# Performance work log

Hardware: AMD Instinct MI355X
Metric: run time of the kernel (lower is better)

## Reference

```python
import jax, jax.numpy as jnp
import numpy as np

NUM_HEADS = 16

def setup_inputs() -> dict:
    key = jax.random.key(0)
    k1, k2, k3 = jax.random.split(key, 3)
    B, T, C = 4, 2048, 2048
    x = jax.random.normal(k1, (B, T, C), dtype=jnp.float32)
    Wqkv = jax.random.normal(k2, (C, 3 * C), dtype=jnp.float32) * (C ** -0.5)
    bqkv = jnp.zeros((3 * C,), dtype=jnp.float32)
    Wproj = jax.random.normal(k3, (C, C), dtype=jnp.float32) * (C ** -0.5)
    bproj = jnp.zeros((C,), dtype=jnp.float32)
    return {"x": x, "Wqkv": Wqkv, "bqkv": bqkv, "Wproj": Wproj, "bproj": bproj}

def reference(x, Wqkv, bqkv, Wproj, bproj):
    B, T, C = x.shape
    H = NUM_HEADS
    D = C // H  # head_dim
    qkv = x @ Wqkv + bqkv                      # [B,T,3C]
    q, k, v = jnp.split(qkv, 3, axis=-1)
    # [B,T,C] -> [B,H,T,D]
    q = q.reshape(B, T, H, D).transpose(0, 2, 1, 3)
    k = k.reshape(B, T, H, D).transpose(0, 2, 1, 3)
    v = v.reshape(B, T, H, D).transpose(0, 2, 1, 3)
    scale = D ** -0.5
    scores = jnp.einsum('bhqd,bhkd->bhqk', q, k) * scale  # [B,H,T,T]
    causal = jnp.tril(jnp.ones((T, T), dtype=bool))
    scores = jnp.where(causal, scores, jnp.finfo(scores.dtype).min)
    attn = jax.nn.softmax(scores, axis=-1)
    out = jnp.einsum('bhqk,bhkd->bhqd', attn, v)           # [B,H,T,D]
    out = out.transpose(0, 2, 1, 3).reshape(B, T, C)
    return out @ Wproj + bproj
```

## Files before the change

### kernel.cpp

```cpp
#include <hip/hip_runtime.h>
#include <hip/hip_bf16.h>
#include <stdint.h>

typedef __attribute__((ext_vector_type(8))) short short8;
typedef __attribute__((ext_vector_type(4))) float f32x4;
typedef __attribute__((ext_vector_type(16))) float f32x16;
typedef __attribute__((ext_vector_type(2))) unsigned int uint2v;

__device__ __forceinline__ unsigned short f2bf(float f) {
  union { float f; unsigned int u; } v; v.f = f;
  unsigned int r = v.u + 0x7FFFu + ((v.u >> 16) & 1u);
  return (unsigned short)(r >> 16);
}

__device__ __forceinline__ unsigned int cvtpk(float lo, float hi) {
  unsigned int r;
  asm("v_cvt_pk_bf16_f32 %0, %1, %2" : "=v"(r) : "v"(lo), "v"(hi));
  return r;
}

#define GLOAD16(gsrc, ldst)                                                                  \
  __builtin_amdgcn_global_load_lds((const __attribute__((address_space(1))) void*)(gsrc),    \
                                   (__attribute__((address_space(3))) void*)(ldst), 16, 0, 0)

#define BAR() __builtin_amdgcn_s_barrier()
#define LGKMC(n) do { asm volatile("s_waitcnt lgkmcnt(" #n ")" ::: "memory"); \
                      __builtin_amdgcn_sched_barrier(0); } while (0)
#define LGKM0() LGKMC(0)
#define VMCNT0() asm volatile("s_waitcnt vmcnt(0)" ::: "memory")
#define VMCNT8() do { asm volatile("s_waitcnt vmcnt(8)" ::: "memory"); \
                      __builtin_amdgcn_sched_barrier(0); } while (0)
#define PRIO(x) __builtin_amdgcn_s_setprio(x)
#define MFMA16(d, a, b) d = __builtin_amdgcn_mfma_f32_16x16x32_bf16(a, b, d, 0, 0, 0)

__global__ __launch_bounds__(256) void cast_bf16_kernel(const float* __restrict__ in,
                                                        unsigned short* __restrict__ out) {
  int i = blockIdx.x * 256 + threadIdx.x;
  float4 v = ((const float4*)in)[i];
  ushort4 o;
  o.x = f2bf(v.x); o.y = f2bf(v.y); o.z = f2bf(v.z); o.w = f2bf(v.w);
  ((ushort4*)out)[i] = o;
}

__global__ __launch_bounds__(256) void transpose_cast_kernel(const float* __restrict__ W,
                                                             unsigned short* __restrict__ Wt,
                                                             int K, int N) {
  __shared__ float tile[32][33];
  int n0 = blockIdx.x * 32, k0 = blockIdx.y * 32;
  int tx = threadIdx.x, ty = threadIdx.y;
#pragma unroll
  for (int j = 0; j < 32; j += 8)
    tile[ty + j][tx] = W[(size_t)(k0 + ty + j) * N + n0 + tx];
  __syncthreads();
#pragma unroll
  for (int j = 0; j < 32; j += 8)
    Wt[(size_t)(n0 + ty + j) * K + k0 + tx] = f2bf(tile[tx][ty + j]);
}

__device__ __forceinline__ void stage_half(const unsigned short* __restrict__ gp, int K,
                                           int kt, int half, char* lds_mat, int tid) {
#pragma unroll
  for (int it = 0; it < 2; ++it) {
    int li = half * 1024 + it * 512 + tid;
    int r = li >> 3, c = li & 7;
    int cs = c ^ (r & 7);
    GLOAD16(gp + (size_t)r * K + kt * 64 + cs * 8, lds_mat + li * 16);
  }
}

__device__ __forceinline__ void gemm256_mainloop(const unsigned short* __restrict__ Ap,
                                                 const unsigned short* __restrict__ Bp,
                                                 int K, int tid, char* smem,
                                                 f32x4 acc[8][4]) {
  char* sa = smem;
  char* sb = smem + 65536;
  const int KT = K >> 6;

  int wid = tid >> 6, lane = tid & 63;
  int wr = wid >> 2, wc = wid & 3;
  int lg = lane >> 4, l15 = lane & 15;
  int swz7 = l15 & 7;

#define LDA(ab, m, kc) \
  (*(const short8*)((const unsigned short*)(ab) + (size_t)((wr * 128 + (m) * 16 + l15) * 64 + ((((kc) * 4 + lg) ^ swz7) * 8))))
#define LDB(bb, n, kc) \
  (*(const short8*)((const unsigned short*)(bb) + (size_t)((wc * 64 + (n) * 16 + l15) * 64 + ((((kc) * 4 + lg) ^ swz7) * 8))))

  stage_half(Bp, K, 0, 0, sb, tid);
  stage_half(Bp, K, 0, 1, sb, tid);
  stage_half(Ap, K, 0, 0, sa, tid);
  stage_half(Ap, K, 0, 1, sa, tid);
  stage_half(Bp, K, 1, 0, sb + 32768, tid);
  stage_half(Bp, K, 1, 1, sb + 32768, tid);
  stage_half(Ap, K, 1, 0, sa + 32768, tid);
  stage_half(Ap, K, 1, 1, sa + 32768, tid);
  VMCNT8();
  BAR();

  for (int t = 0; t < KT; ++t) {
    int p = t & 1;
    const char* ab = sa + p * 32768;
    const char* bb = sb + p * 32768;
    int kt2 = (t + 2 < KT) ? t + 2 : KT - 1;

    short8 bq01[2][2], bq23[2][2], aq[4][2], aq2[4][2];
#pragma unroll
    for (int n = 0; n < 2; ++n) { bq01[n][0] = LDB(bb, n, 0); bq01[n][1] = LDB(bb, n, 1); }
#pragma unroll
    for (int m = 0; m < 4; ++m) { aq[m][0] = LDA(ab, m, 0); aq[m][1] = LDA(ab, m, 1); }
#pragma unroll
    for (int n = 0; n < 2; ++n) { bq23[n][0] = LDB(bb, n + 2, 0); bq23[n][1] = LDB(bb, n + 2, 1); }
#pragma unroll
    for (int m = 0; m < 4; ++m) { aq2[m][0] = LDA(ab, m + 4, 0); aq2[m][1] = LDA(ab, m + 4, 1); }

    LGKMC(12);
    PRIO(1);
#pragma unroll
    for (int kc = 0; kc < 2; ++kc)
#pragma unroll
      for (int m = 0; m < 4; ++m)
#pragma unroll
        for (int n = 0; n < 2; ++n)
          MFMA16(acc[m][n], aq[m][kc], bq01[n][kc]);
    PRIO(0);

    LGKMC(8);
    BAR();
    stage_half(Bp, K, kt2, 0, sb + p * 32768, tid);
    stage_half(Bp, K, kt2, 1, sb + p * 32768, tid);

    PRIO(1);
#pragma unroll
    for (int kc = 0; kc < 2; ++kc)
#pragma unroll
      for (int m = 0; m < 4; ++m)
#pragma unroll
        for (int n = 0; n < 2; ++n)
          MFMA16(acc[m][n + 2], aq[m][kc], bq23[n][kc]);
    PRIO(0);

    LGKMC(0);
    PRIO(1);
#pragma unroll
    for (int kc = 0; kc < 2; ++kc)
#pragma unroll
      for (int m = 0; m < 4; ++m)
#pragma unroll
        for (int n = 0; n < 2; ++n)
          MFMA16(acc[m + 4][n + 2], aq2[m][kc], bq23[n][kc]);
    PRIO(0);

    BAR();
    stage_half(Ap, K, kt2, 0, sa + p * 32768, tid);
    stage_half(Ap, K, kt2, 1, sa + p * 32768, tid);
    PRIO(1);
#pragma unroll
    for (int kc = 0; kc < 2; ++kc)
#pragma unroll
      for (int m = 0; m < 4; ++m)
#pragma unroll
        for (int n = 0; n < 2; ++n)
          MFMA16(acc[m + 4][n], aq2[m][kc], bq01[n][kc]);
    PRIO(0);
    VMCNT8();
    BAR();
  }
#undef LDA
#undef LDB
}

__global__ __launch_bounds__(512, 2) void gemm_qkv256_kernel(const unsigned short* __restrict__ A,
                                                             const unsigned short* __restrict__ Bt,
                                                             const float* __restrict__ bias,
                                                             unsigned short* __restrict__ qb,
                                                             unsigned short* __restrict__ kb,
                                                             unsigned short* __restrict__ vtb) {
  extern __shared__ char smem[];
  int wg = blockIdx.x;
  int xcd = wg & 7, idx = wg >> 3;
  int bn = xcd * 3 + idx % 3;
  int bm = idx / 3;
  int tid = threadIdx.x;

  f32x4 acc[8][4];
  f32x4 zero = {0.f, 0.f, 0.f, 0.f};
#pragma unroll
  for (int m = 0; m < 8; ++m)
#pragma unroll
    for (int n = 0; n < 4; ++n) acc[m][n] = zero;

  gemm256_mainloop(A + (size_t)bm * 256 * 2048, Bt + (size_t)bn * 256 * 2048, 2048, tid, smem, acc);

  const float QSCALE = (float)(0.08838834764831845 * 1.4426950408889634);
  int wid = tid >> 6, lane = tid & 63;
  int wr = wid >> 2, wc = wid & 3, lg = lane >> 4, l15 = lane & 15;
  int l31 = lane & 31, hi = lane >> 5;

  if (bn >= 16) {
    VMCNT0();
    BAR();
#pragma unroll
    for (int n = 0; n < 4; ++n) {
      int cl = wc * 64 + n * 16 + l15;
      float bv = bias[bn * 256 + cl];
#pragma unroll
      for (int m = 0; m < 8; ++m) {
        int rl = wr * 128 + m * 16 + lg * 4;
        unsigned int w0 = cvtpk(acc[m][n][0] + bv, acc[m][n][1] + bv);
        unsigned int w1 = cvtpk(acc[m][n][2] + bv, acc[m][n][3] + bv);
        uint2v pk = {w0, w1};
        *(uint2v*)(smem + cl * 512 + ((rl * 2) ^ ((cl & 7) << 4))) = pk;
      }
    }
    LGKM0();
    BAR();
    int t0_abs = bm * 256;
    int bq_ = t0_abs >> 11, t0 = t0_abs & 2047;
    int h0 = (bn * 256 - 4096) >> 7;
#pragma unroll
    for (int i = 0; i < 16; ++i) {
      int dloc = i * 16 + wid * 2 + hi;
      short8 vrow = *(const short8*)(smem + dloc * 512 + ((l31 * 16) ^ ((dloc & 7) << 4)));
      int bh_ = bq_ * 16 + h0 + (dloc >> 7);
      int d = dloc & 127;
      *(short8*)(vtb + ((size_t)bh_ * 128 + d) * 2048 + t0 + l31 * 8) = vrow;
    }
  } else {
#pragma unroll
    for (int n = 0; n < 4; ++n) {
      int col = bn * 256 + wc * 64 + n * 16 + l15;
      float bv = bias[col];
      int which = col >> 11;
      int h = (col & 2047) >> 7;
      int d = col & 127;
#pragma unroll
      for (int m = 0; m < 8; ++m) {
#pragma unroll
        for (int g = 0; g < 4; ++g) {
          int row = bm * 256 + wr * 128 + m * 16 + lg * 4 + g;
          int b = row >> 11, t = row & 2047;
          float r = acc[m][n][g] + bv;
          if (which == 0) r *= QSCALE;
          unsigned short val = f2bf(r);
          size_t bhi = (size_t)(b * 16 + h);
          if (which == 0) qb[(bhi * 2048 + t) * 128 + d] = val;
          else            kb[(bhi * 2048 + t) * 128 + d] = val;
        }
      }
    }
  }
}

__global__ __launch_bounds__(512, 2) void gemm_proj256_kernel(const unsigned short* __restrict__ A,
                                                              const unsigned short* __restrict__ Bt,
                                                              const float* __restrict__ bias,
                                                              float* __restrict__ out) {
  extern __shared__ char smem[];
  int wg = blockIdx.x;
  int bm = wg >> 3, bn = wg & 7;
  int tid = threadIdx.x;

  f32x4 acc[8][4];
  f32x4 zero = {0.f, 0.f, 0.f, 0.f};
#pragma unroll
  for (int m = 0; m < 8; ++m)
#pragma unroll
    for (int n = 0; n < 4; ++n) acc[m][n] = zero;

  gemm256_mainloop(A + (size_t)bm * 256 * 2048, Bt + (size_t)bn * 256 * 2048, 2048, tid, smem, acc);

  int wid = tid >> 6, lane = tid & 63;
  int wr = wid >> 2, wc = wid & 3, lg = lane >> 4, l15 = lane & 15;
#pragma unroll
  for (int n = 0; n < 4; ++n) {
    int col = bn * 256 + wc * 64 + n * 16 + l15;
    float bv = bias[col];
#pragma unroll
    for (int m = 0; m < 8; ++m) {
#pragma unroll
      for (int g = 0; g < 4; ++g) {
        int row = bm * 256 + wr * 128 + m * 16 + lg * 4 + g;
        out[(size_t)row * 2048 + col] = acc[m][n][g] + bv;
      }
    }
  }
}

__global__ __launch_bounds__(512) void attn_kernel(const unsigned short* __restrict__ qb,
                                                   const unsigned short* __restrict__ kb,
                                                   const unsigned short* __restrict__ vtb,
                                                   unsigned short* __restrict__ ob) {
  extern __shared__ char asmem[];
  int pairi = blockIdx.x;
  int bh = blockIdx.y;
  int b = bh >> 4, h = bh & 15;
  int tid = threadIdx.x, wid = tid >> 6, lane = tid & 63;
  int l31 = lane & 31, hi = lane >> 5;

  const unsigned short* Q  = qb  + (size_t)bh * 2048 * 128;
  const unsigned short* K  = kb  + (size_t)bh * 2048 * 128;
  const unsigned short* Vt = vtb + (size_t)bh * 128 * 2048;

#pragma unroll 1
  for (int pass = 0; pass < 2; ++pass) {
    int qt = pass == 0 ? (7 - pairi) : pairi;
    int NT = 4 * qt + 4;
    int qbase = qt * 256 + wid * 32;
    int qrow = qbase + l31;

    short8 qf[8];
#pragma unroll
    for (int kc = 0; kc < 8; ++kc)
      qf[kc] = *(const short8*)(Q + (size_t)qrow * 128 + kc * 16 + hi * 8);

    f32x16 o0 = {}, o1 = {}, o2 = {}, o3 = {};
    float m_run = -1e30f, l_run = 0.f;

    {
      char* kb_ = asmem;
#pragma unroll
      for (int it = 0; it < 2; ++it) {
        int li = it * 512 + tid;
        int r = li >> 4, c = li & 15;
        GLOAD16(K + (size_t)r * 128 + (c ^ (r & 7)) * 8, kb_ + li * 16);
      }
#pragma unroll
      for (int it = 0; it < 2; ++it) {
        int li = it * 512 + tid;
        int r = li >> 3, c = li & 7;
        GLOAD16(Vt + (size_t)r * 2048 + (c ^ (r & 7)) * 8, kb_ + 16384 + li * 16);
      }
    }
    VMCNT0();
    BAR();

#pragma unroll 1
    for (int kt = 0; kt < NT; ++kt) {
      char* cb = asmem + ((kt & 1) << 15);
      if (kt + 1 < NT) {
        char* nb = asmem + (((kt + 1) & 1) << 15);
        int kt1 = kt + 1;
#pragma unroll
        for (int it = 0; it < 2; ++it) {
          int li = it * 512 + tid;
          int r = li >> 4, c = li & 15;
          GLOAD16(K + (size_t)(kt1 * 64 + r) * 128 + (c ^ (r & 7)) * 8, nb + li * 16);
        }
#pragma unroll
        for (int it = 0; it < 2; ++it) {
          int li = it * 512 + tid;
          int r = li >> 3, c = li & 7;
          GLOAD16(Vt + (size_t)r * 2048 + kt1 * 64 + (c ^ (r & 7)) * 8, nb + 16384 + li * 16);
        }
      }

      bool active = (kt * 64 <= qbase + 31);
      if (active) {
        const char* k_l = cb;
        const char* v_l = cb + 16384;

        f32x16 s0v = {}, s1v = {};
        PRIO(1);
#pragma unroll
        for (int kc = 0; kc < 8; ++kc) {
          int cg = kc * 2 + hi;
          int sw = l31 & 7;
          short8 kf0 = *(const short8*)(k_l + l31 * 256 + ((cg ^ sw) * 16));
          s0v = __builtin_amdgcn_mfma_f32_32x32x16_bf16(kf0, qf[kc], s0v, 0, 0, 0);
          short8 kf1 = *(const short8*)(k_l + (32 + l31) * 256 + ((cg ^ sw) * 16));
          s1v = __builtin_amdgcn_mfma_f32_32x32x16_bf16(kf1, qf[kc], s1v, 0, 0, 0);
        }
        PRIO(0);

        if (kt * 64 + 63 > qbase) {
          int kvb = kt * 64 + 4 * hi;
#pragma unroll
          for (int r = 0; r < 16; ++r) {
            int kv = kvb + (r & 3) + 8 * (r >> 2);
            if (kv > qrow) s0v[r] = -1e30f;
            if (kv + 32 > qrow) s1v[r] = -1e30f;
          }
        }

        float tmax[16];
#pragma unroll
        for (int i = 0; i < 16; ++i) tmax[i] = fmaxf(s0v[i], s1v[i]);
#pragma unroll
        for (int st = 8; st >= 1; st >>= 1)
#pragma unroll
          for (int i = 0; i < st; ++i) tmax[i] = fmaxf(tmax[i], tmax[i + st]);
        float pmax = fmaxf(tmax[0], __shfl_xor(tmax[0], 32));

        if (!__all(pmax <= m_run + 8.0f)) {
          float mn = fmaxf(m_run, pmax);
          float alpha = exp2f(m_run - mn);
          m_run = mn; l_run *= alpha;
          o0 *= alpha; o1 *= alpha; o2 *= alpha; o3 *= alpha;
        }

#pragma unroll
        for (int i = 0; i < 16; ++i) {
          s0v[i] = exp2f(s0v[i] - m_run);
          s1v[i] = exp2f(s1v[i] - m_run);
        }
        float tsum[16];
#pragma unroll
        for (int i = 0; i < 16; ++i) tsum[i] = s0v[i] + s1v[i];
#pragma unroll
        for (int st = 8; st >= 1; st >>= 1)
#pragma unroll
          for (int i = 0; i < st; ++i) tsum[i] += tsum[i + st];
        float rsum = tsum[0] + __shfl_xor(tsum[0], 32);
        l_run += rsum;

#define BUILD_PA(sv, base, out)                                                \
        {                                                                      \
          unsigned int a_ = cvtpk(sv[base + 0], sv[base + 1]);                 \
          unsigned int c_ = cvtpk(sv[base + 2], sv[base + 3]);                 \
          unsigned int b_ = cvtpk(sv[base + 4], sv[base + 5]);                 \
          unsigned int d_ = cvtpk(sv[base + 6], sv[base + 7]);                 \
          uint2v r0_ = __builtin_amdgcn_permlane32_swap(a_, b_, false, false); \
          uint2v r1_ = __builtin_amdgcn_permlane32_swap(c_, d_, false, false); \
          union { unsigned int u[4]; short8 v; } uu_;                          \
          uu_.u[0] = r0_[0]; uu_.u[1] = r1_[0]; uu_.u[2] = r0_[1]; uu_.u[3] = r1_[1]; \
          out = uu_.v;                                                         \
        }
        short8 pa0, pa1, pa2, pa3;
        BUILD_PA(s0v, 0, pa0);
        BUILD_PA(s0v, 8, pa1);
        BUILD_PA(s1v, 0, pa2);
        BUILD_PA(s1v, 8, pa3);
#undef BUILD_PA

        PRIO(1);
#define PV_STEP(ovar, dt)                                                          \
        {                                                                          \
          int rv_ = dt * 32 + l31;                                                 \
          const char* vb_ = v_l + rv_ * 128;                                       \
          int sw_ = rv_ & 7;                                                       \
          short8 v0_ = *(const short8*)(vb_ + (((0 + hi) ^ sw_) * 16));            \
          ovar = __builtin_amdgcn_mfma_f32_32x32x16_bf16(v0_, pa0, ovar, 0, 0, 0); \
          short8 v1_ = *(const short8*)(vb_ + (((2 + hi) ^ sw_) * 16));            \
          ovar = __builtin_amdgcn_mfma_f32_32x32x16_bf16(v1_, pa1, ovar, 0, 0, 0); \
          short8 v2_ = *(const short8*)(vb_ + (((4 + hi) ^ sw_) * 16));            \
          ovar = __builtin_amdgcn_mfma_f32_32x32x16_bf16(v2_, pa2, ovar, 0, 0, 0); \
          short8 v3_ = *(const short8*)(vb_ + (((6 + hi) ^ sw_) * 16));            \
          ovar = __builtin_amdgcn_mfma_f32_32x32x16_bf16(v3_, pa3, ovar, 0, 0, 0); \
        }
        PV_STEP(o0, 0)
        PV_STEP(o1, 1)
        PV_STEP(o2, 2)
        PV_STEP(o3, 3)
#undef PV_STEP
        PRIO(0);
      }

      VMCNT0();
      BAR();
    }

    float inv = 1.0f / l_run;
    size_t orow = (size_t)(b * 2048 + qt * 256 + wid * 32 + l31);
    unsigned short* ob_p = ob + orow * 2048 + h * 128;
#define STORE_DT(ovar, dt)                                                         \
    {                                                                              \
      _Pragma("unroll")                                                            \
      for (int rq = 0; rq < 4; ++rq) {                                             \
        unsigned int w0 = cvtpk(ovar[rq * 4 + 0] * inv, ovar[rq * 4 + 1] * inv);   \
        unsigned int w1 = cvtpk(ovar[rq * 4 + 2] * inv, ovar[rq * 4 + 3] * inv);   \
        uint2v st = {w0, w1};                                                      \
        *(uint2v*)(ob_p + dt * 32 + rq * 8 + 4 * hi) = st;                         \
      }                                                                            \
    }
    STORE_DT(o0, 0)
    STORE_DT(o1, 1)
    STORE_DT(o2, 2)
    STORE_DT(o3, 3)
#undef STORE_DT
  }
}

extern "C" void kernel_launch(void* const* d_in, const int* in_sizes, int n_in,
                              void* d_out, int out_size, void* d_ws, size_t ws_size,
                              hipStream_t stream) {
  const float* x     = (const float*)d_in[0];
  const float* Wqkv  = (const float*)d_in[1];
  const float* bqkv  = (const float*)d_in[2];
  const float* Wproj = (const float*)d_in[3];
  const float* bproj = (const float*)d_in[4];
  float* out = (float*)d_out;

  char* ws = (char*)d_ws;
  unsigned short* x_bf   = (unsigned short*)ws;
  unsigned short* wqkvt  = (unsigned short*)(ws + 33554432);
  unsigned short* wprojt = (unsigned short*)(ws + 33554432 + 25165824);
  unsigned short* qb     = (unsigned short*)(ws + 67108864);
  unsigned short* kb     = (unsigned short*)(ws + 100663296);
  unsigned short* vtb    = (unsigned short*)(ws + 134217728);

  (void)hipFuncSetAttribute((const void*)gemm_qkv256_kernel,
                            hipFuncAttributeMaxDynamicSharedMemorySize, 131072);
  (void)hipFuncSetAttribute((const void*)gemm_proj256_kernel,
                            hipFuncAttributeMaxDynamicSharedMemorySize, 131072);
  (void)hipFuncSetAttribute((const void*)attn_kernel,
                            hipFuncAttributeMaxDynamicSharedMemorySize, 65536);

  cast_bf16_kernel<<<16384, 256, 0, stream>>>(x, x_bf);
  transpose_cast_kernel<<<dim3(192, 64), dim3(32, 8), 0, stream>>>(Wqkv, wqkvt, 2048, 6144);
  transpose_cast_kernel<<<dim3(64, 64), dim3(32, 8), 0, stream>>>(Wproj, wprojt, 2048, 2048);
  gemm_qkv256_kernel<<<768, 512, 131072, stream>>>(x_bf, wqkvt, bqkv, qb, kb, vtb);
  attn_kernel<<<dim3(4, 64), 512, 65536, stream>>>(qb, kb, vtb, x_bf );
  gemm_proj256_kernel<<<256, 512, 131072, stream>>>(x_bf, wprojt, bproj, out);
}
```

Baseline: 408.3 us.

## Reschedule GEMM mainloop: B tile one stage ahead, A two ahead, finer barriers

Restructures the 256-tile GEMM mainloop's prefetch schedule. B is now prefetched only one k-step ahead into the other buffer, while A stays two steps ahead. Loads and MFMA quadrants are interleaved in four phases with barriers and full LDS waits between them, and the vmcnt threshold drops from 8 to 4. The aim is to spread global-to-LDS traffic more evenly across the iteration, at the cost of more barriers per k-step and shorter register lookahead.

Result: no change. 412.6 us (+1.0%).

```diff
diff --git a/kernel.cpp b/kernel.cpp
--- a/kernel.cpp
+++ b/kernel.cpp
@@ -28,7 +28,7 @@
                       __builtin_amdgcn_sched_barrier(0); } while (0)
 #define LGKM0() LGKMC(0)
 #define VMCNT0() asm volatile("s_waitcnt vmcnt(0)" ::: "memory")
-#define VMCNT8() do { asm volatile("s_waitcnt vmcnt(8)" ::: "memory"); \
+#define VMCNT4() do { asm volatile("s_waitcnt vmcnt(4)" ::: "memory"); \
                       __builtin_amdgcn_sched_barrier(0); } while (0)
 #define PRIO(x) __builtin_amdgcn_s_setprio(x)
 #define MFMA16(d, a, b) d = __builtin_amdgcn_mfma_f32_16x16x32_bf16(a, b, d, 0, 0, 0)
@@ -86,34 +86,64 @@
 #define LDB(bb, n, kc) \
   (*(const short8*)((const unsigned short*)(bb) + (size_t)((wc * 64 + (n) * 16 + l15) * 64 + ((((kc) * 4 + lg) ^ swz7) * 8))))
 
+  stage_half(Ap, K, 0, 0, sa, tid);
+  stage_half(Ap, K, 0, 1, sa, tid);
   stage_half(Bp, K, 0, 0, sb, tid);
   stage_half(Bp, K, 0, 1, sb, tid);
-  stage_half(Ap, K, 0, 0, sa, tid);
-  stage_half(Ap, K, 0, 1, sa, tid);
-  stage_half(Bp, K, 1, 0, sb + 32768, tid);
-  stage_half(Bp, K, 1, 1, sb + 32768, tid);
   stage_half(Ap, K, 1, 0, sa + 32768, tid);
   stage_half(Ap, K, 1, 1, sa + 32768, tid);
-  VMCNT8();
+  VMCNT4();
   BAR();
 
   for (int t = 0; t < KT; ++t) {
-    int p = t & 1;
+    int p = t & 1, pn = p ^ 1;
     const char* ab = sa + p * 32768;
     const char* bb = sb + p * 32768;
+    int ktn = (t + 1 < KT) ? t + 1 : KT - 1;
     int kt2 = (t + 2 < KT) ? t + 2 : KT - 1;
 
-    short8 bq01[2][2], bq23[2][2], aq[4][2], aq2[4][2];
+    short8 bq01[2][2], bq23[2][2], aq03[4][2], aq47[4][2];
+
 #pragma unroll
     for (int n = 0; n < 2; ++n) { bq01[n][0] = LDB(bb, n, 0); bq01[n][1] = LDB(bb, n, 1); }
 #pragma unroll
-    for (int m = 0; m < 4; ++m) { aq[m][0] = LDA(ab, m, 0); aq[m][1] = LDA(ab, m, 1); }
+    for (int m = 0; m < 4; ++m) { aq03[m][0] = LDA(ab, m, 0); aq03[m][1] = LDA(ab, m, 1); }
+    stage_half(Bp, K, ktn, 0, sb + pn * 32768, tid);
+    LGKMC(8);
+    BAR();
+    LGKM0();
+    PRIO(1);
+#pragma unroll
+    for (int kc = 0; kc < 2; ++kc)
+#pragma unroll
+      for (int m = 0; m < 4; ++m)
+#pragma unroll
+        for (int n = 0; n < 2; ++n)
+          MFMA16(acc[m][n], aq03[m][kc], bq01[n][kc]);
+    PRIO(0);
+    BAR();
+
+#pragma unroll
+    for (int m = 0; m < 4; ++m) { aq47[m][0] = LDA(ab, m + 4, 0); aq47[m][1] = LDA(ab, m + 4, 1); }
+    stage_half(Bp, K, ktn, 1, sb + pn * 32768, tid);
+    BAR();
+    LGKM0();
+    PRIO(1);
+#pragma unroll
+    for (int kc = 0; kc < 2; ++kc)
+#pragma unroll
+      for (int m = 0; m < 4; ++m)
+#pragma unroll
+        for (int n = 0; n < 2; ++n)
+          MFMA16(acc[m + 4][n], aq47[m][kc], bq01[n][kc]);
+    PRIO(0);
+    BAR();
+
 #pragma unroll
     for (int n = 0; n < 2; ++n) { bq23[n][0] = LDB(bb, n + 2, 0); bq23[n][1] = LDB(bb, n + 2, 1); }
-#pragma unroll
-    for (int m = 0; m < 4; ++m) { aq2[m][0] = LDA(ab, m + 4, 0); aq2[m][1] = LDA(ab, m + 4, 1); }
-
-    LGKMC(12);
+    stage_half(Ap, K, kt2, 0, sa + p * 32768, tid);
+    BAR();
+    LGKM0();
     PRIO(1);
 #pragma unroll
     for (int kc = 0; kc < 2; ++kc)
@@ -121,14 +151,13 @@
       for (int m = 0; m < 4; ++m)
 #pragma unroll
         for (int n = 0; n < 2; ++n)
-          MFMA16(acc[m][n], aq[m][kc], bq01[n][kc]);
+          MFMA16(acc[m + 4][n + 2], aq47[m][kc], bq23[n][kc]);
     PRIO(0);
-
-    LGKMC(8);
-    BAR();
-    stage_half(Bp, K, kt2, 0, sb + p * 32768, tid);
-    stage_half(Bp, K, kt2, 1, sb + p * 32768, tid);
-
+    BAR();
+
+    stage_half(Ap, K, kt2, 1, sa + p * 32768, tid);
+    VMCNT4();
+    BAR();
     PRIO(1);
 #pragma unroll
     for (int kc = 0; kc < 2; ++kc)
@@ -136,33 +165,8 @@
       for (int m = 0; m < 4; ++m)
 #pragma unroll
         for (int n = 0; n < 2; ++n)
-          MFMA16(acc[m][n + 2], aq[m][kc], bq23[n][kc]);
+          MFMA16(acc[m][n + 2], aq03[m][kc], bq23[n][kc]);
     PRIO(0);
-
-    LGKMC(0);
-    PRIO(1);
-#pragma unroll
-    for (int kc = 0; kc < 2; ++kc)
-#pragma unroll
-      for (int m = 0; m < 4; ++m)
-#pragma unroll
-        for (int n = 0; n < 2; ++n)
-          MFMA16(acc[m + 4][n + 2], aq2[m][kc], bq23[n][kc]);
-    PRIO(0);
-
-    BAR();
-    stage_half(Ap, K, kt2, 0, sa + p * 32768, tid);
-    stage_half(Ap, K, kt2, 1, sa + p * 32768, tid);
-    PRIO(1);
-#pragma unroll
-    for (int kc = 0; kc < 2; ++kc)
-#pragma unroll
-      for (int m = 0; m < 4; ++m)
-#pragma unroll
-        for (int n = 0; n < 2; ++n)
-          MFMA16(acc[m + 4][n], aq2[m][kc], bq01[n][kc]);
-    PRIO(0);
-    VMCNT8();
     BAR();
   }
 #undef LDA
```
